# Optimization experiments

Measured on AMD Instinct MI355X. Metric: run time of the kernel, lower is better.

Reference implementation:

```python
import jax, jax.numpy as jnp
import numpy as np

USER_COUNT = 100000
ITEM_COUNT = 50000
N_NODES = USER_COUNT + ITEM_COUNT
NNZ = 4800000
EMB = 64
BATCH = 4096


def setup_inputs() -> dict:
    key = jax.random.key(0)
    k1, k2, k3, k4, k5, k6, k7 = jax.random.split(key, 7)
    return {
        "user_emb": jax.random.normal(k1, (USER_COUNT, EMB), dtype=jnp.float32),
        "item_emb": jax.random.normal(k2, (ITEM_COUNT, EMB), dtype=jnp.float32),
        "adj_vals": jax.random.uniform(k3, (NNZ,), dtype=jnp.float32),
        "adj_row": jax.random.randint(k4, (NNZ,), 0, N_NODES, dtype=jnp.int64),
        "adj_col": jax.random.randint(k5, (NNZ,), 0, N_NODES, dtype=jnp.int64),
        "users": jax.random.randint(k6, (BATCH,), 0, USER_COUNT, dtype=jnp.int64),
        "items": jax.random.randint(k7, (BATCH,), 0, ITEM_COUNT, dtype=jnp.int64),
        "n_layers": 3,
    }


def _spmm(adj_row, adj_col, adj_vals, x):
    # sparse (N,N) @ dense (N,D): gather source rows, scale by edge values, scatter-add to dest
    msgs = adj_vals[:, None] * x[adj_col]  # [nnz, D]
    return jax.ops.segment_sum(msgs, adj_row, num_segments=N_NODES)


def reference(user_emb, item_emb, adj_vals, adj_row, adj_col, users, items, n_layers):
    ego = jnp.concatenate([user_emb, item_emb], axis=0)  # [N, D]
    for _ in range(n_layers):
        ego = _spmm(adj_row, adj_col, adj_vals, ego)
    user_all = ego[:USER_COUNT]
    item_all = ego[USER_COUNT:]
    return (user_all[users], item_all[items])
```

## Files before the change

### kernel.cpp

```cpp
#include <hip/hip_runtime.h>
#include <hip/hip_bf16.h>

#define USER_COUNT 100000
#define ITEM_COUNT 50000
#define N_NODES    150000
#define EMB        64
#define BATCH      4096

#define NFINE      586
#define FSHIFT     8
#define STRIDE     8960
#define TILE_E     6400
#define NBSTRIDE   768

__device__ inline unsigned short f2bf_raw(float f) {
    __hip_bfloat16 h = __float2bfloat16(f);
    unsigned short u; __builtin_memcpy(&u, &h, 2); return u;
}

__global__ __launch_bounds__(512) void count_kernel(
        const int* __restrict__ rows, int* __restrict__ counts, int nnz) {
    __shared__ int cnt[NFINE];
    const int b = blockIdx.x, t = threadIdx.x;
    for (int f = t; f < NFINE; f += 512) cnt[f] = 0;
    __syncthreads();
    const int s = b * TILE_E, e = min(s + TILE_E, nnz);
    for (int i = s + t; i < e; i += 512)
        atomicAdd(&cnt[rows[i] >> FSHIFT], 1);
    __syncthreads();
    for (int f = t; f < NFINE; f += 512)
        counts[f * NBSTRIDE + b] = cnt[f];
}

__global__ __launch_bounds__(1024) void scan_offs(
        const int* __restrict__ counts, int* __restrict__ offs,
        int* __restrict__ tot, int nblk) {
    __shared__ int s[1024];
    const int f = blockIdx.x, t = threadIdx.x;
    const int c = (t < nblk) ? counts[f * NBSTRIDE + t] : 0;
    s[t] = c;
    __syncthreads();
    for (int o = 1; o < 1024; o <<= 1) {
        int v = (t >= o) ? s[t - o] : 0;
        __syncthreads();
        s[t] += v;
        __syncthreads();
    }
    if (t < nblk) offs[f * NBSTRIDE + t] = s[t] - c;
    if (t == 1023) tot[f] = s[1023];
}

__global__ __launch_bounds__(512) void partition_kernel(
        const float* __restrict__ vals,
        const int* __restrict__ rows,
        const int* __restrict__ cols,
        const int* __restrict__ offs,
        uint2* __restrict__ fine, int nnz) {
    __shared__ uint2 buf[TILE_E];
    __shared__ int   cnt[NFINE];
    __shared__ int   sloff[NFINE + 1];
    __shared__ int   gb[NFINE];
    __shared__ int   sscan[512];
    const int b = blockIdx.x, t = threadIdx.x;
    const int sbeg = b * TILE_E, send = min(sbeg + TILE_E, nnz);
    const int n = send - sbeg;

    for (int f = t; f < NFINE; f += 512) {
        cnt[f] = 0;
        gb[f] = f * STRIDE + offs[f * NBSTRIDE + b];
    }
    __syncthreads();
    for (int i = sbeg + t; i < send; i += 512)
        atomicAdd(&cnt[rows[i] >> FSHIFT], 1);
    __syncthreads();
    int c0 = (2 * t < NFINE) ? cnt[2 * t] : 0;
    int c1 = (2 * t + 1 < NFINE) ? cnt[2 * t + 1] : 0;
    sscan[t] = c0 + c1;
    __syncthreads();
    for (int o = 1; o < 512; o <<= 1) {
        int v = (t >= o) ? sscan[t - o] : 0;
        __syncthreads();
        sscan[t] += v;
        __syncthreads();
    }
    int base = (t == 0) ? 0 : sscan[t - 1];
    if (2 * t < NFINE) sloff[2 * t] = base;
    if (2 * t + 1 < NFINE) sloff[2 * t + 1] = base + c0;
    if (t == 511) sloff[NFINE] = sscan[511];
    __syncthreads();
    for (int f = t; f < NFINE; f += 512) cnt[f] = sloff[f];
    __syncthreads();
    for (int i = sbeg + t; i < send; i += 512) {
        int r = rows[i];
        int f = r >> FSHIFT;
        int pos = atomicAdd(&cnt[f], 1);
        buf[pos] = make_uint2(__float_as_uint(vals[i]),
                              (unsigned)cols[i] | ((unsigned)(r & 255) << 18));
    }
    __syncthreads();
    for (int idx = t; idx < n; idx += 512) {
        int lo = 0, hi = NFINE;
        while (hi - lo > 1) {
            int mid = (lo + hi) >> 1;
            if (sloff[mid] <= idx) lo = mid; else hi = mid;
        }
        fine[gb[lo] + (idx - sloff[lo])] = buf[idx];
    }
}

__global__ __launch_bounds__(256) void bucket_sort_kernel(
        const uint2* __restrict__ fine,
        const int* __restrict__ tot,
        float2* __restrict__ perm,
        uint2* __restrict__ rp) {
    __shared__ int hist[256];
    __shared__ int off[256];
    __shared__ int cur[256];
    const int f    = blockIdx.x;
    const int tid  = threadIdx.x;
    const int n    = min(tot[f], STRIDE);
    const int base = f * STRIDE;
    const uint2* src = fine + base;

    hist[tid] = 0;
    __syncthreads();
    for (int k = tid; k < n; k += 256)
        atomicAdd(&hist[(src[k].y >> 18) & 255], 1);
    __syncthreads();
    if (tid == 0) {
        int acc = 0;
        for (int j = 0; j < 256; ++j) { off[j] = acc; acc += hist[j]; }
    }
    __syncthreads();
    cur[tid] = off[tid];
    int row = (f << FSHIFT) + tid;
    if (row < N_NODES)
        rp[row] = make_uint2(base + off[tid], base + off[tid] + hist[tid]);
    __syncthreads();
    for (int k = tid; k < n; k += 256) {
        uint2 e = src[k];
        int lrow = (e.y >> 18) & 255;
        int pos = base + atomicAdd(&cur[lrow], 1);
        perm[pos] = make_float2(__uint_as_float(e.x),
                                __int_as_float((int)(e.y & 0x3FFFFu)));
    }
}

__global__ void to_bf16(const float4* __restrict__ ue,
                        const float4* __restrict__ ie,
                        uint2* __restrict__ xh) {
    int i = blockIdx.x * blockDim.x + threadIdx.x;
    const int n4 = (N_NODES * EMB) / 4;
    const int u4 = (USER_COUNT * EMB) / 4;
    if (i >= n4) return;
    float4 fv = (i < u4) ? ue[i] : ie[i - u4];
    uint2 o;
    o.x = (unsigned int)f2bf_raw(fv.x) | ((unsigned int)f2bf_raw(fv.y) << 16);
    o.y = (unsigned int)f2bf_raw(fv.z) | ((unsigned int)f2bf_raw(fv.w) << 16);
    xh[i] = o;
}

#define ACC8(U, W)                                      \
    a0 += (W) * __uint_as_float((U).x << 16);           \
    a1 += (W) * __uint_as_float((U).x & 0xffff0000u);   \
    a2 += (W) * __uint_as_float((U).y << 16);           \
    a3 += (W) * __uint_as_float((U).y & 0xffff0000u);   \
    a4 += (W) * __uint_as_float((U).z << 16);           \
    a5 += (W) * __uint_as_float((U).z & 0xffff0000u);   \
    a6 += (W) * __uint_as_float((U).w << 16);           \
    a7 += (W) * __uint_as_float((U).w & 0xffff0000u);

__global__ void spmm_bf16(const uint2* __restrict__ rp,
                          const float2* __restrict__ perm,
                          const unsigned short* __restrict__ xh,
                          unsigned short* __restrict__ yh) {
    int wid  = (blockIdx.x * blockDim.x + threadIdx.x) >> 6;
    int lane = threadIdx.x & 63;
    int g    = lane >> 3;
    int s    = lane & 7;
    int r    = (wid << 3) + g;
    if (r >= N_NODES) return;

    uint2 be = rp[r];
    int beg = (int)be.x, end = (int)be.y;

    const uint4* xv = (const uint4*)xh;
    float a0 = 0.f, a1 = 0.f, a2 = 0.f, a3 = 0.f;
    float a4 = 0.f, a5 = 0.f, a6 = 0.f, a7 = 0.f;

    int j = beg;
    for (; j + 7 < end; j += 8) {
        float2 e0 = perm[j];
        float2 e1 = perm[j + 1];
        float2 e2 = perm[j + 2];
        float2 e3 = perm[j + 3];
        float2 e4 = perm[j + 4];
        float2 e5 = perm[j + 5];
        float2 e6 = perm[j + 6];
        float2 e7 = perm[j + 7];
        uint4 u0 = xv[(((long long)__float_as_int(e0.y)) << 3) + s];
        uint4 u1 = xv[(((long long)__float_as_int(e1.y)) << 3) + s];
        uint4 u2 = xv[(((long long)__float_as_int(e2.y)) << 3) + s];
        uint4 u3 = xv[(((long long)__float_as_int(e3.y)) << 3) + s];
        uint4 u4 = xv[(((long long)__float_as_int(e4.y)) << 3) + s];
        uint4 u5 = xv[(((long long)__float_as_int(e5.y)) << 3) + s];
        uint4 u6 = xv[(((long long)__float_as_int(e6.y)) << 3) + s];
        uint4 u7 = xv[(((long long)__float_as_int(e7.y)) << 3) + s];
        ACC8(u0, e0.x) ACC8(u1, e1.x) ACC8(u2, e2.x) ACC8(u3, e3.x)
        ACC8(u4, e4.x) ACC8(u5, e5.x) ACC8(u6, e6.x) ACC8(u7, e7.x)
    }
    for (; j < end; ++j) {
        float2 e = perm[j];
        uint4 u = xv[(((long long)__float_as_int(e.y)) << 3) + s];
        ACC8(u, e.x)
    }

    uint4 o;
    o.x = (unsigned)f2bf_raw(a0) | ((unsigned)f2bf_raw(a1) << 16);
    o.y = (unsigned)f2bf_raw(a2) | ((unsigned)f2bf_raw(a3) << 16);
    o.z = (unsigned)f2bf_raw(a4) | ((unsigned)f2bf_raw(a5) << 16);
    o.w = (unsigned)f2bf_raw(a6) | ((unsigned)f2bf_raw(a7) << 16);
    ((uint4*)yh)[(((long long)r) << 3) + s] = o;
}

__global__ void spmm_batch_kernel(const uint2* __restrict__ rp,
                                  const float2* __restrict__ perm,
                                  const unsigned short* __restrict__ xh,
                                  const int* __restrict__ users,
                                  const int* __restrict__ items,
                                  float4* __restrict__ out) {
    int wid  = (blockIdx.x * blockDim.x + threadIdx.x) >> 6;
    int lane = threadIdx.x & 63;
    int g    = lane >> 3;
    int s    = lane & 7;
    int b    = (wid << 3) + g;
    if (b >= 2 * BATCH) return;
    int node = (b < BATCH) ? users[b] : (USER_COUNT + items[b - BATCH]);

    uint2 be = rp[node];
    int beg = (int)be.x, end = (int)be.y;

    const uint4* xv = (const uint4*)xh;
    float a0 = 0.f, a1 = 0.f, a2 = 0.f, a3 = 0.f;
    float a4 = 0.f, a5 = 0.f, a6 = 0.f, a7 = 0.f;

    int j = beg;
    for (; j + 3 < end; j += 4) {
        float2 e0 = perm[j];
        float2 e1 = perm[j + 1];
        float2 e2 = perm[j + 2];
        float2 e3 = perm[j + 3];
        uint4 u0 = xv[(((long long)__float_as_int(e0.y)) << 3) + s];
        uint4 u1 = xv[(((long long)__float_as_int(e1.y)) << 3) + s];
        uint4 u2 = xv[(((long long)__float_as_int(e2.y)) << 3) + s];
        uint4 u3 = xv[(((long long)__float_as_int(e3.y)) << 3) + s];
        ACC8(u0, e0.x) ACC8(u1, e1.x) ACC8(u2, e2.x) ACC8(u3, e3.x)
    }
    for (; j < end; ++j) {
        float2 e = perm[j];
        uint4 u = xv[(((long long)__float_as_int(e.y)) << 3) + s];
        ACC8(u, e.x)
    }

    out[(size_t)b * 16 + 2 * s]     = make_float4(a0, a1, a2, a3);
    out[(size_t)b * 16 + 2 * s + 1] = make_float4(a4, a5, a6, a7);
}

extern "C" void kernel_launch(void* const* d_in, const int* in_sizes, int n_in,
                              void* d_out, int out_size, void* d_ws, size_t ws_size,
                              hipStream_t stream) {
    const float* user_emb = (const float*)d_in[0];
    const float* item_emb = (const float*)d_in[1];
    const float* adj_vals = (const float*)d_in[2];
    const int*   adj_row  = (const int*)d_in[3];
    const int*   adj_col  = (const int*)d_in[4];
    const int*   users    = (const int*)d_in[5];
    const int*   items    = (const int*)d_in[6];

    const int nnz  = in_sizes[2];
    const int nblk = (nnz + TILE_E - 1) / TILE_E;

    const size_t region = (size_t)NFINE * STRIDE + 1024;

    char* p = (char*)d_ws;
    uint2* fine = (uint2*)p;
    unsigned short* xh_a = (unsigned short*)p;
    unsigned short* xh_b = xh_a + (size_t)N_NODES * EMB;
    p += region * sizeof(uint2);
    float2* perm = (float2*)p;
    p += region * sizeof(float2);
    uint2* rp = (uint2*)p;
    p += (size_t)(N_NODES + 16) * sizeof(uint2);
    int* counts = (int*)p;  p += (size_t)NFINE * NBSTRIDE * sizeof(int);
    int* offs   = (int*)p;  p += (size_t)NFINE * NBSTRIDE * sizeof(int);
    int* tot    = (int*)p;

    count_kernel<<<nblk, 512, 0, stream>>>(adj_row, counts, nnz);
    scan_offs<<<NFINE, 1024, 0, stream>>>(counts, offs, tot, nblk);
    partition_kernel<<<nblk, 512, 0, stream>>>(adj_vals, adj_row, adj_col,
                                               offs, fine, nnz);
    bucket_sort_kernel<<<NFINE, 256, 0, stream>>>(fine, tot, perm, rp);

    const int n4 = (N_NODES * EMB) / 4;
    to_bf16<<<(n4 + 255) / 256, 256, 0, stream>>>((const float4*)user_emb,
                                                  (const float4*)item_emb,
                                                  (uint2*)xh_a);

    const int spmm_blocks = (N_NODES / 8 + 3) / 4;
    spmm_bf16<<<spmm_blocks, 256, 0, stream>>>(rp, perm, xh_a, xh_b);
    spmm_bf16<<<spmm_blocks, 256, 0, stream>>>(rp, perm, xh_b, xh_a);
    spmm_batch_kernel<<<(2 * BATCH / 8) / 4, 256, 0, stream>>>(
        rp, perm, xh_a, users, items, (float4*)d_out);
}
```

Baseline: 440.8 us.

## Sort edges within each row by column segment and reduce gather unroll

The bucket sort now bins edges by destination row and by column segment (16K-column ranges), using a parallel scan in place of a serial one, so edges within each row are ordered by source-column region. This is meant to improve cache locality of the gathered bf16 rows across rows processed concurrently in the SpMM. The SpMM inner loop unroll drops from 8 to 4, which lowers register pressure and may raise occupancy but leaves fewer loads in flight per thread. The sort kernel needs more shared memory and more scan synchronisation.

```diff
diff --git a/kernel.cpp b/kernel.cpp
--- a/kernel.cpp
+++ b/kernel.cpp
@@ -12,6 +12,10 @@
 #define STRIDE     8960
 #define TILE_E     6400
 #define NBSTRIDE   768
+
+#define SEGSHIFT   14
+#define NSEG       10
+#define NBINS      (256 * NSEG)
 
 __device__ inline unsigned short f2bf_raw(float f) {
     __hip_bfloat16 h = __float2bfloat16(f);
@@ -113,36 +117,54 @@
         const int* __restrict__ tot,
         float2* __restrict__ perm,
         uint2* __restrict__ rp) {
-    __shared__ int hist[256];
-    __shared__ int off[256];
-    __shared__ int cur[256];
+    __shared__ int off[NBINS + 1];
+    __shared__ int cur[NBINS];
+    __shared__ int sscan[256];
     const int f    = blockIdx.x;
     const int tid  = threadIdx.x;
     const int n    = min(tot[f], STRIDE);
     const int base = f * STRIDE;
     const uint2* src = fine + base;
 
-    hist[tid] = 0;
-    __syncthreads();
-    for (int k = tid; k < n; k += 256)
-        atomicAdd(&hist[(src[k].y >> 18) & 255], 1);
-    __syncthreads();
-    if (tid == 0) {
-        int acc = 0;
-        for (int j = 0; j < 256; ++j) { off[j] = acc; acc += hist[j]; }
-    }
-    __syncthreads();
-    cur[tid] = off[tid];
-    int row = (f << FSHIFT) + tid;
-    if (row < N_NODES)
-        rp[row] = make_uint2(base + off[tid], base + off[tid] + hist[tid]);
+    for (int k = tid; k < NBINS; k += 256) cur[k] = 0;
     __syncthreads();
     for (int k = tid; k < n; k += 256) {
         uint2 e = src[k];
         int lrow = (e.y >> 18) & 255;
-        int pos = base + atomicAdd(&cur[lrow], 1);
-        perm[pos] = make_float2(__uint_as_float(e.x),
-                                __int_as_float((int)(e.y & 0x3FFFFu)));
+        int seg  = (int)((e.y & 0x3FFFFu) >> SEGSHIFT);
+        atomicAdd(&cur[lrow * NSEG + seg], 1);
+    }
+    __syncthreads();
+    int local[NSEG];
+    int s = 0;
+    #pragma unroll
+    for (int q = 0; q < NSEG; ++q) { local[q] = cur[tid * NSEG + q]; s += local[q]; }
+    sscan[tid] = s;
+    __syncthreads();
+    for (int o = 1; o < 256; o <<= 1) {
+        int v = (tid >= o) ? sscan[tid - o] : 0;
+        __syncthreads();
+        sscan[tid] += v;
+        __syncthreads();
+    }
+    int run = (tid == 0) ? 0 : sscan[tid - 1];
+    #pragma unroll
+    for (int q = 0; q < NSEG; ++q) { off[tid * NSEG + q] = run; run += local[q]; }
+    if (tid == 255) off[NBINS] = run;
+    __syncthreads();
+    int row = (f << FSHIFT) + tid;
+    if (row < N_NODES)
+        rp[row] = make_uint2(base + off[tid * NSEG],
+                             base + off[(tid + 1) * NSEG]);
+    for (int k = tid; k < NBINS; k += 256) cur[k] = off[k];
+    __syncthreads();
+    for (int k = tid; k < n; k += 256) {
+        uint2 e = src[k];
+        int lrow = (e.y >> 18) & 255;
+        unsigned col = e.y & 0x3FFFFu;
+        int seg = (int)(col >> SEGSHIFT);
+        int pos = base + atomicAdd(&cur[lrow * NSEG + seg], 1);
+        perm[pos] = make_float2(__uint_as_float(e.x), __int_as_float((int)col));
     }
 }
 
@@ -189,25 +211,16 @@
     float a4 = 0.f, a5 = 0.f, a6 = 0.f, a7 = 0.f;
 
     int j = beg;
-    for (; j + 7 < end; j += 8) {
+    for (; j + 3 < end; j += 4) {
         float2 e0 = perm[j];
         float2 e1 = perm[j + 1];
         float2 e2 = perm[j + 2];
         float2 e3 = perm[j + 3];
-        float2 e4 = perm[j + 4];
-        float2 e5 = perm[j + 5];
-        float2 e6 = perm[j + 6];
-        float2 e7 = perm[j + 7];
         uint4 u0 = xv[(((long long)__float_as_int(e0.y)) << 3) + s];
         uint4 u1 = xv[(((long long)__float_as_int(e1.y)) << 3) + s];
         uint4 u2 = xv[(((long long)__float_as_int(e2.y)) << 3) + s];
         uint4 u3 = xv[(((long long)__float_as_int(e3.y)) << 3) + s];
-        uint4 u4 = xv[(((long long)__float_as_int(e4.y)) << 3) + s];
-        uint4 u5 = xv[(((long long)__float_as_int(e5.y)) << 3) + s];
-        uint4 u6 = xv[(((long long)__float_as_int(e6.y)) << 3) + s];
-        uint4 u7 = xv[(((long long)__float_as_int(e7.y)) << 3) + s];
         ACC8(u0, e0.x) ACC8(u1, e1.x) ACC8(u2, e2.x) ACC8(u3, e3.x)
-        ACC8(u4, e4.x) ACC8(u5, e5.x) ACC8(u6, e6.x) ACC8(u7, e7.x)
     }
     for (; j < end; ++j) {
         float2 e = perm[j];
```

Result: slower. 453.5 us (+2.9%).
